# Kernel tuning notes

Hardware: AMD Instinct MI355X
Metric: run time of the kernel (lower is better)

Reference implementation:

```python
import jax, jax.numpy as jnp
import numpy as np

N, D, H, C, E = 16384, 768, 768, 2, 20

def setup_inputs() -> dict:
    key = jax.random.key(0)
    k1, k2, k3, k4, k5, k6 = jax.random.split(key, 6)
    return {
        "embeddings": jax.random.normal(k1, (N, D), dtype=jnp.float32),
        "component_idx": jax.random.randint(k2, (N,), 0, E, dtype=jnp.int64),
        "W1": jax.random.normal(k3, (E, D, H), dtype=jnp.float32) * (1.0 / np.sqrt(D)),
        "b1": jnp.zeros((E, H), dtype=jnp.float32),
        "W2": jax.random.normal(k4, (E, H, C), dtype=jnp.float32) * (1.0 / np.sqrt(H)),
        "b2": jnp.zeros((E, C), dtype=jnp.float32),
    }

def reference(embeddings, component_idx, W1, b1, W2, b2):
    # Each token n goes through expert component_idx[n]:
    #   y = relu(x @ W1[e] + b1[e]) @ W2[e] + b2[e]
    # The torch module's mask/cat/argsort reassembly is mathematically a
    # per-token select of its own expert's output at the original position.
    # Dense-expert formulation (standard jax MoE fallback), then gather.
    h = jax.nn.relu(jnp.einsum('nd,edh->enh', embeddings, W1) + b1[:, None, :])  # [E,N,H]
    y = jnp.einsum('enh,ehc->enc', h, W2) + b2[:, None, :]                        # [E,N,C]
    n_idx = jnp.arange(embeddings.shape[0])
    return y[component_idx, n_idx]  # [N,C]
```

## Files before the change

kernel.cpp:

```cpp
#include <hip/hip_runtime.h>

#define N_D 768
#define N_H 768
#define N_C 2
#define N_E 20
#define MT 128
#define NT 128
#define BK 32
#define KT (N_D / BK)
#define MAX_TILES 160

typedef __attribute__((ext_vector_type(8))) short short8;
typedef __attribute__((ext_vector_type(4))) float f32x4;

__device__ __forceinline__ unsigned short f2bf(float f) {
  unsigned u = __builtin_bit_cast(unsigned, f);
  u += 0x7FFFu + ((u >> 16) & 1u);
  return (unsigned short)(u >> 16);
}

#define GLD_LDS16(gp, lp)                                                        \
  __builtin_amdgcn_global_load_lds(                                              \
      (const __attribute__((address_space(1))) void*)(gp),                       \
      (__attribute__((address_space(3))) void*)(lp), 16, 0, 0)


__global__ __launch_bounds__(256) void k_hist(const int* __restrict__ cidx,
                                              int* __restrict__ counts, int n) {
  __shared__ int lc[N_E];
  if (threadIdx.x < N_E) lc[threadIdx.x] = 0;
  __syncthreads();
  for (int i = blockIdx.x * blockDim.x + threadIdx.x; i < n;
       i += gridDim.x * blockDim.x) {
    int e = cidx[i];
    e = e < 0 ? 0 : (e >= N_E ? N_E - 1 : e);
    atomicAdd(&lc[e], 1);
  }
  __syncthreads();
  if (threadIdx.x < N_E) atomicAdd(&counts[threadIdx.x], lc[threadIdx.x]);
}

__global__ void k_scan(const int* __restrict__ counts, int* __restrict__ offsets,
                       int* __restrict__ cursor, int* __restrict__ tiles,
                       int* __restrict__ numTiles) {
  if (threadIdx.x == 0) {
    int run = 0, t = 0;
    for (int e = 0; e < N_E; ++e) {
      offsets[e] = run;
      cursor[e] = run;
      int nt = (counts[e] + MT - 1) / MT;
      for (int m = 0; m < nt && t < MAX_TILES; ++m) tiles[t++] = (e << 8) | m;
      run += counts[e];
    }
    *numTiles = t;
  }
}

__global__ __launch_bounds__(256) void k_scatter(const int* __restrict__ cidx,
                                                 int* __restrict__ cursor,
                                                 int* __restrict__ sorted, int n) {
  __shared__ int lc[N_E];
  __shared__ int lbase[N_E];
  int tid = threadIdx.x;
  if (tid < N_E) lc[tid] = 0;
  __syncthreads();
  int i = blockIdx.x * blockDim.x + tid;
  int e = 0, p = 0;
  if (i < n) {
    e = cidx[i];
    e = e < 0 ? 0 : (e >= N_E ? N_E - 1 : e);
    p = atomicAdd(&lc[e], 1);
  }
  __syncthreads();
  if (tid < N_E) lbase[tid] = atomicAdd(&cursor[tid], lc[tid]);
  __syncthreads();
  if (i < n) sorted[lbase[e] + p] = i;
}


__global__ __launch_bounds__(192) void k_gather(const float* __restrict__ emb,
                                                const int* __restrict__ sorted,
                                                unsigned short* __restrict__ Xg,
                                                int n) {
  int row = blockIdx.x;
  int j = threadIdx.x;
  ushort4 o;
  if (row < n) {
    float4 v = ((const float4*)(emb + (size_t)sorted[row] * N_D))[j];
    o.x = f2bf(v.x);
    o.y = f2bf(v.y);
    o.z = f2bf(v.z);
    o.w = f2bf(v.w);
  } else {
    o.x = o.y = o.z = o.w = 0;
  }
  ((ushort4*)(Xg + (size_t)row * N_D))[j] = o;
}


__global__ __launch_bounds__(256) void k_w1_cvt(const float* __restrict__ W1,
                                                unsigned short* __restrict__ W1t) {
  __shared__ float tile[64][65];
  int e = blockIdx.z, h0 = blockIdx.x * 64, d0 = blockIdx.y * 64;
  const float* src = W1 + (size_t)e * N_D * N_H;
  unsigned short* dst = W1t + (size_t)e * N_H * N_D;
  int tx = threadIdx.x & 15, ty = threadIdx.x >> 4;
  for (int s = 0; s < 4; ++s) {
    int d = s * 16 + ty;
    float4 v = *(const float4*)&src[(size_t)(d0 + d) * N_H + h0 + tx * 4];
    tile[d][tx * 4 + 0] = v.x;
    tile[d][tx * 4 + 1] = v.y;
    tile[d][tx * 4 + 2] = v.z;
    tile[d][tx * 4 + 3] = v.w;
  }
  __syncthreads();
  int px = threadIdx.x & 7, py = threadIdx.x >> 3;
  for (int s = 0; s < 2; ++s) {
    int h = s * 32 + py;
    short8 v;
    for (int j = 0; j < 8; ++j)
      v[j] = (short)f2bf(tile[px * 8 + j][h]);
    *(short8*)&dst[(size_t)(h0 + h) * N_D + d0 + px * 8] = v;
  }
}


__global__ __launch_bounds__(256, 2) void k_gemm(
    const unsigned short* __restrict__ Xg, const unsigned short* __restrict__ W1t,
    const float* __restrict__ b1, const float* __restrict__ W2,
    const float* __restrict__ b2, const int* __restrict__ sorted,
    const int* __restrict__ counts, const int* __restrict__ offsets,
    const int* __restrict__ tiles, const int* __restrict__ numTiles,
    float* __restrict__ out) {
  if ((int)blockIdx.y >= *numTiles) return;
  const int tv = tiles[blockIdx.y];
  const int e = tv >> 8;
  const int m0 = (tv & 255) * MT;
  const int off = offsets[e];
  const int cnt_rel = counts[e] - m0;
  const int n0 = blockIdx.x * NT;

  __shared__ unsigned short lA[2][MT * BK];
  __shared__ unsigned short lB[2][NT * BK];

  const int tid = threadIdx.x;
  const int wid = tid >> 6, lane = tid & 63;
  const int wm = (wid >> 1) * 64, wn = (wid & 1) * 64;
  const int quad = lane >> 4, lm = lane & 15;

  const int srow = lane >> 2;
  const int schunk = (lane & 3) ^ (srow & 3);
  const unsigned short* ag =
      Xg + (size_t)(off + m0 + wid * 32 + srow) * N_D + schunk * 8;
  const unsigned short* bg = W1t + (size_t)e * N_H * N_D +
                             (size_t)(n0 + wid * 32 + srow) * N_D + schunk * 8;
  unsigned short* lAw0 = &lA[0][(wid * 32) * BK];
  unsigned short* lAw1 = &lA[1][(wid * 32) * BK];
  unsigned short* lBw0 = &lB[0][(wid * 32) * BK];
  unsigned short* lBw1 = &lB[1][(wid * 32) * BK];

  const int koff = (quad ^ (lm & 3)) * 8;

  f32x4 acc[4][4] = {};

  {
    GLD_LDS16(ag, lAw0);
    GLD_LDS16(ag + 16 * N_D, lAw0 + 16 * BK);
    GLD_LDS16(bg, lBw0);
    GLD_LDS16(bg + 16 * N_D, lBw0 + 16 * BK);
  }

  for (int kt = 0; kt < KT; ++kt) {
    const int cur = kt & 1;
    __syncthreads();
    if (kt + 1 < KT) {
      const unsigned short* agk = ag + (kt + 1) * BK;
      const unsigned short* bgk = bg + (kt + 1) * BK;
      unsigned short* la = cur ? lAw0 : lAw1;
      unsigned short* lb = cur ? lBw0 : lBw1;
      GLD_LDS16(agk, la);
      GLD_LDS16(agk + 16 * N_D, la + 16 * BK);
      GLD_LDS16(bgk, lb);
      GLD_LDS16(bgk + 16 * N_D, lb + 16 * BK);
    }
    short8 af[4], bfr[4];
    for (int i = 0; i < 4; ++i)
      af[i] = *(const short8*)&lA[cur][(wm + i * 16 + lm) * BK + koff];
    for (int j = 0; j < 4; ++j)
      bfr[j] = *(const short8*)&lB[cur][(wn + j * 16 + lm) * BK + koff];
    for (int i = 0; i < 4; ++i)
      for (int j = 0; j < 4; ++j)
        acc[i][j] =
            __builtin_amdgcn_mfma_f32_16x16x32_bf16(af[i], bfr[j], acc[i][j], 0, 0, 0);
  }

  float y0[4][4], y1[4][4];
  for (int i = 0; i < 4; ++i)
    for (int r = 0; r < 4; ++r) y0[i][r] = y1[i][r] = 0.f;

  for (int j = 0; j < 4; ++j) {
    int col = n0 + wn + j * 16 + lm;
    float bias = b1[e * N_H + col];
    float2 w2 = *(const float2*)&W2[((size_t)e * N_H + col) * N_C];
    for (int i = 0; i < 4; ++i) {
      f32x4 a = acc[i][j];
      for (int r = 0; r < 4; ++r) {
        float h = a[r] + bias;
        h = h > 0.f ? h : 0.f;
        y0[i][r] += h * w2.x;
        y1[i][r] += h * w2.y;
      }
    }
  }
  for (int s = 1; s < 16; s <<= 1) {
    for (int i = 0; i < 4; ++i)
      for (int r = 0; r < 4; ++r) {
        y0[i][r] += __shfl_xor(y0[i][r], s, 64);
        y1[i][r] += __shfl_xor(y1[i][r], s, 64);
      }
  }
  if (lm == 0) {
    const bool add_bias = (n0 == 0) && (wn == 0);
    float bb0 = add_bias ? b2[e * N_C + 0] : 0.f;
    float bb1 = add_bias ? b2[e * N_C + 1] : 0.f;
    for (int i = 0; i < 4; ++i) {
      for (int r = 0; r < 4; ++r) {
        int mrel = wm + i * 16 + quad * 4 + r;
        if (mrel < cnt_rel) {
          int token = sorted[off + m0 + mrel];
          atomicAdd(&out[(size_t)token * N_C + 0], y0[i][r] + bb0);
          atomicAdd(&out[(size_t)token * N_C + 1], y1[i][r] + bb1);
        }
      }
    }
  }
}


extern "C" void kernel_launch(void* const* d_in, const int* in_sizes, int n_in,
                              void* d_out, int out_size, void* d_ws, size_t ws_size,
                              hipStream_t stream) {
  const float* emb = (const float*)d_in[0];
  const int* cidx = (const int*)d_in[1];
  const float* W1 = (const float*)d_in[2];
  const float* b1 = (const float*)d_in[3];
  const float* W2 = (const float*)d_in[4];
  const float* b2 = (const float*)d_in[5];
  float* out = (float*)d_out;
  const int n = in_sizes[1];

  char* ws = (char*)d_ws;
  int* counts = (int*)ws;
  int* offsets = (int*)(ws + 128);
  int* cursor = (int*)(ws + 256);
  int* numTiles = (int*)(ws + 384);
  int* tiles = (int*)(ws + 512);
  int* sorted = (int*)(ws + 2048);
  size_t sorted_bytes = ((size_t)n * 4 + 255) & ~(size_t)255;
  unsigned short* Xg = (unsigned short*)(ws + 2048 + sorted_bytes);
  int pcap = n + MT;
  unsigned short* W1t = Xg + (size_t)pcap * N_D;

  hipMemsetAsync(d_ws, 0, 2048, stream);
  hipMemsetAsync(d_out, 0, (size_t)out_size * sizeof(float), stream);
  int nb = (n + 255) / 256;
  k_hist<<<nb, 256, 0, stream>>>(cidx, counts, n);
  k_scan<<<1, 64, 0, stream>>>(counts, offsets, cursor, tiles, numTiles);
  k_scatter<<<nb, 256, 0, stream>>>(cidx, cursor, sorted, n);
  k_gather<<<pcap, 192, 0, stream>>>(emb, sorted, Xg, n);
  k_w1_cvt<<<dim3(N_H / 64, N_D / 64, N_E), 256, 0, stream>>>(W1, W1t);
  k_gemm<<<dim3(N_H / NT, MAX_TILES), 256, 0, stream>>>(
      Xg, W1t, b1, W2, b2, sorted, counts, offsets, tiles, numTiles, out);
}
```

Measured before the change: 223.5 us.

## Deepen GEMM prefetch to two stages with manual waitcnt and fragment-ordered LDS layout

```diff
diff --git a/kernel.cpp b/kernel.cpp
--- a/kernel.cpp
+++ b/kernel.cpp
@@ -9,6 +9,7 @@
 #define BK 32
 #define KT (N_D / BK)
 #define MAX_TILES 160
+#define ROWB (N_D * 2)
 
 typedef __attribute__((ext_vector_type(8))) short short8;
 typedef __attribute__((ext_vector_type(4))) float f32x4;
@@ -148,46 +149,42 @@
   const int wm = (wid >> 1) * 64, wn = (wid & 1) * 64;
   const int quad = lane >> 4, lm = lane & 15;
 
-  const int srow = lane >> 2;
-  const int schunk = (lane & 3) ^ (srow & 3);
-  const unsigned short* ag =
-      Xg + (size_t)(off + m0 + wid * 32 + srow) * N_D + schunk * 8;
-  const unsigned short* bg = W1t + (size_t)e * N_H * N_D +
-                             (size_t)(n0 + wid * 32 + srow) * N_D + schunk * 8;
-  unsigned short* lAw0 = &lA[0][(wid * 32) * BK];
-  unsigned short* lAw1 = &lA[1][(wid * 32) * BK];
-  unsigned short* lBw0 = &lB[0][(wid * 32) * BK];
-  unsigned short* lBw1 = &lB[1][(wid * 32) * BK];
-
-  const int koff = (quad ^ (lm & 3)) * 8;
+  const int R0 = wid * 32 + lm;
+  const char* agp = (const char*)Xg + (size_t)(off + m0 + R0) * ROWB + quad * 16;
+  const char* bgp = (const char*)W1t + (size_t)e * N_H * ROWB +
+                    (size_t)(n0 + R0) * ROWB + quad * 16;
+  unsigned short* lap[2] = {&lA[0][(wid * 32) * BK], &lA[1][(wid * 32) * BK]};
+  unsigned short* lbp[2] = {&lB[0][(wid * 32) * BK], &lB[1][(wid * 32) * BK]};
+
+#define ISSUE_BATCH(kk, b)                                                       \
+  do {                                                                           \
+    const char* a_ = agp + (kk)*64;                                              \
+    const char* b_ = bgp + (kk)*64;                                              \
+    GLD_LDS16(a_, lap[b]);                                                       \
+    GLD_LDS16(a_ + 16 * ROWB, lap[b] + 16 * BK);                                 \
+    GLD_LDS16(b_, lbp[b]);                                                       \
+    GLD_LDS16(b_ + 16 * ROWB, lbp[b] + 16 * BK);                                 \
+  } while (0)
 
   f32x4 acc[4][4] = {};
 
-  {
-    GLD_LDS16(ag, lAw0);
-    GLD_LDS16(ag + 16 * N_D, lAw0 + 16 * BK);
-    GLD_LDS16(bg, lBw0);
-    GLD_LDS16(bg + 16 * N_D, lBw0 + 16 * BK);
-  }
+  ISSUE_BATCH(0, 0);
+  ISSUE_BATCH(1, 1);
+
+  const int fa = quad * 128 + lm * 8;
 
   for (int kt = 0; kt < KT; ++kt) {
     const int cur = kt & 1;
-    __syncthreads();
-    if (kt + 1 < KT) {
-      const unsigned short* agk = ag + (kt + 1) * BK;
-      const unsigned short* bgk = bg + (kt + 1) * BK;
-      unsigned short* la = cur ? lAw0 : lAw1;
-      unsigned short* lb = cur ? lBw0 : lBw1;
-      GLD_LDS16(agk, la);
-      GLD_LDS16(agk + 16 * N_D, la + 16 * BK);
-      GLD_LDS16(bgk, lb);
-      GLD_LDS16(bgk + 16 * N_D, lb + 16 * BK);
-    }
+    asm volatile("s_waitcnt vmcnt(4)\n\ts_barrier" ::: "memory");
     short8 af[4], bfr[4];
     for (int i = 0; i < 4; ++i)
-      af[i] = *(const short8*)&lA[cur][(wm + i * 16 + lm) * BK + koff];
+      af[i] = *(const short8*)&lA[cur][((wm >> 4) + i) * 512 + fa];
     for (int j = 0; j < 4; ++j)
-      bfr[j] = *(const short8*)&lB[cur][(wn + j * 16 + lm) * BK + koff];
+      bfr[j] = *(const short8*)&lB[cur][((wn >> 4) + j) * 512 + fa];
+    asm volatile("s_waitcnt lgkmcnt(0)\n\ts_barrier" ::: "memory");
+    int kk = kt + 2;
+    if (kk >= KT) kk -= KT;
+    ISSUE_BATCH(kk, cur);
     for (int i = 0; i < 4; ++i)
       for (int j = 0; j < 4; ++j)
         acc[i][j] =
```

After: 222.5 us. No clear change (-0.4%).
